# Kernel optimization log

Hardware: AMD Instinct MI355X
Metric: run time of the kernel (lower is better)

The kernel has to match this reference:

```python
import jax, jax.numpy as jnp
import numpy as np

N_BOND = 100000      # number of 'bond' nodes in the batched graph
IN_DIM = 32
SPACE_NUM = 6
D = SPACE_NUM * IN_DIM  # 192; bo_merge='cat' keeps h at space_num*in_dim
N_ETYPES = 36        # len(prot_atom_ids) * len(drug_atom_ids) = 4 * 9
E_PER_TYPE = 30000   # edges per edge type
B = 256              # batch_size (number of graphs)


def setup_inputs() -> dict:
    key = jax.random.key(0)
    k1, k2, k3, k4, k5 = jax.random.split(key, 5)
    h = jax.random.normal(k1, (N_BOND, D), dtype=jnp.float32)
    # output_layer: nn.Linear(D, 1, bias=False)
    W_out = jax.random.normal(k2, (D, 1), dtype=jnp.float32) / np.sqrt(D)
    # per-edge-type source node ids (DGL copy_u gather indices)
    edge_src = jax.random.randint(k3, (N_ETYPES, E_PER_TYPE), 0, N_BOND, dtype=jnp.int32)
    # per-edge graph id; sorted within each type (mimics arange(B).repeat(batch_num_edges))
    edge_seg = jnp.sort(jax.random.randint(k4, (N_ETYPES, E_PER_TYPE), 0, B, dtype=jnp.int32), axis=1)
    mask_mat = jax.random.randint(k5, (B, N_ETYPES), 0, 2).astype(bool)
    return {"h": h, "W_out": W_out, "edge_src": edge_src,
            "edge_seg": edge_seg, "mask_mat": mask_mat}


def reference(h, W_out, edge_src, edge_seg, mask_mat):
    # Fused over all 36 edge types: global segment id = type * B + graph_id
    type_idx = jnp.arange(N_ETYPES, dtype=edge_seg.dtype)[:, None]        # [T,1]
    seg_global = (type_idx * B + edge_seg).reshape(-1)                    # [T*E]
    eh = h[edge_src.reshape(-1)]                                          # gather: [T*E, D]
    sums = jax.ops.segment_sum(eh, seg_global, num_segments=N_ETYPES * B)  # [T*B, D]
    graph_feat = sums.reshape(N_ETYPES, B, D).transpose(1, 0, 2)          # [B, T, D]
    graph_v = jnp.einsum('btd,do->bt', graph_feat, W_out)                 # [B, T]
    graph_v = jnp.where(mask_mat, jnp.float32(-1e9), graph_v)
    return jax.nn.softmax(graph_v, axis=1)
```

## Files before the change

### kernel.cpp

```cpp
#include <hip/hip_runtime.h>

#define N_BOND   100000
#define D_DIM    192
#define N_ETYPES 36
#define E_PER_TYPE 30000
#define BATCH    256
#define TOTAL_E  (N_ETYPES * E_PER_TYPE)

__global__ void hv_kernel(const float* __restrict__ h, const float* __restrict__ W,
                          float* __restrict__ hv) {
    int gwave = (blockIdx.x * blockDim.x + threadIdx.x) >> 6;
    int lane  = threadIdx.x & 63;
    if (gwave >= N_BOND) return;
    float v = 0.f;
    if (lane < 48) {
        const float4 a = ((const float4*)(h + (size_t)gwave * D_DIM))[lane];
        const float4 w = ((const float4*)W)[lane];
        v = a.x * w.x + a.y * w.y + a.z * w.z + a.w * w.w;
    }
#pragma unroll
    for (int d = 32; d > 0; d >>= 1) v += __shfl_down(v, d, 64);
    if (lane == 0) hv[gwave] = v;
}

__global__ void edge_kernel(const int* __restrict__ edge_src,
                            const int* __restrict__ edge_seg,
                            const float* __restrict__ hv,
                            float* __restrict__ acc) {
    int e    = blockIdx.x * blockDim.x + threadIdx.x;
    int lane = threadIdx.x & 63;
    bool valid = (e < TOTAL_E);
    int ec  = valid ? e : (TOTAL_E - 1);
    int t   = ec / E_PER_TYPE;
    int seg = edge_seg[ec];
    int src = edge_src[ec];
    float val = valid ? hv[src] : 0.0f;
    int key = t * BATCH + seg;

#pragma unroll
    for (int d = 1; d < 64; d <<= 1) {
        float uv = __shfl_up(val, d, 64);
        int   uk = __shfl_up(key, d, 64);
        if (lane >= d && uk == key) val += uv;
    }
    int nk = __shfl_down(key, 1, 64);
    if (lane == 63 || nk != key) atomicAdd(&acc[key], val);
}

__global__ void softmax_kernel(const float* __restrict__ acc,
                               const void* __restrict__ mask,
                               float* __restrict__ out) {
    int b = threadIdx.x;

    const unsigned int* mi = (const unsigned int*)mask;
    bool is_u8 = false;
#pragma unroll
    for (int i = 0; i < 16; ++i) is_u8 |= (mi[i] > 1u);
    const unsigned char* m8  = (const unsigned char*)mask;
    const int*           m32 = (const int*)mask;

    float v[N_ETYPES];
    float mx = -1e30f;
#pragma unroll
    for (int t = 0; t < N_ETYPES; ++t) {
        float x = acc[t * BATCH + b];
        bool masked = is_u8 ? (m8[b * N_ETYPES + t] != 0)
                            : (m32[b * N_ETYPES + t] != 0);
        x = masked ? -1e9f : x;
        v[t] = x;
        mx = fmaxf(mx, x);
    }
    float s = 0.f;
#pragma unroll
    for (int t = 0; t < N_ETYPES; ++t) { v[t] = expf(v[t] - mx); s += v[t]; }
    float inv = 1.f / s;
#pragma unroll
    for (int t = 0; t < N_ETYPES; ++t) out[b * N_ETYPES + t] = v[t] * inv;
}

extern "C" void kernel_launch(void* const* d_in, const int* in_sizes, int n_in,
                              void* d_out, int out_size, void* d_ws, size_t ws_size,
                              hipStream_t stream) {
    const float* h        = (const float*)d_in[0];
    const float* W        = (const float*)d_in[1];
    const int*   edge_src = (const int*)d_in[2];
    const int*   edge_seg = (const int*)d_in[3];
    const void*  mask     = d_in[4];
    float*       out      = (float*)d_out;

    float* hv  = (float*)d_ws;
    float* acc = (float*)((char*)d_ws + 400128);

    hipMemsetAsync(acc, 0, N_ETYPES * BATCH * sizeof(float), stream);

    hipLaunchKernelGGL(hv_kernel, dim3((N_BOND + 3) / 4), dim3(256), 0, stream, h, W, hv);

    int eb = (TOTAL_E + 255) / 256;
    hipLaunchKernelGGL(edge_kernel, dim3(eb), dim3(256), 0, stream, edge_src, edge_seg, hv, acc);

    hipLaunchKernelGGL(softmax_kernel, dim3(1), dim3(256), 0, stream, acc, mask, out);
}
```

Before: 140.8 us.

## Fold acc zeroing into hv kernel and process 8 edges per thread serially

```diff
diff --git a/kernel.cpp b/kernel.cpp
--- a/kernel.cpp
+++ b/kernel.cpp
@@ -6,45 +6,51 @@
 #define E_PER_TYPE 30000
 #define BATCH    256
 #define TOTAL_E  (N_ETYPES * E_PER_TYPE)
+#define EPT      8
 
 __global__ void hv_kernel(const float* __restrict__ h, const float* __restrict__ W,
-                          float* __restrict__ hv) {
-    int gwave = (blockIdx.x * blockDim.x + threadIdx.x) >> 6;
-    int lane  = threadIdx.x & 63;
-    if (gwave >= N_BOND) return;
-    float v = 0.f;
-    if (lane < 48) {
-        const float4 a = ((const float4*)(h + (size_t)gwave * D_DIM))[lane];
-        const float4 w = ((const float4*)W)[lane];
-        v = a.x * w.x + a.y * w.y + a.z * w.z + a.w * w.w;
-    }
+                          float* __restrict__ hv, float* __restrict__ acc) {
+    int gid  = blockIdx.x * blockDim.x + threadIdx.x;
+    if (gid < N_ETYPES * BATCH) acc[gid] = 0.f;
+    int row  = gid >> 6;
+    int lane = threadIdx.x & 63;
+    if (row >= N_BOND) return;
+    const float* hr = h + (size_t)row * D_DIM;
+    float v = hr[lane]       * W[lane]
+            + hr[lane + 64]  * W[lane + 64]
+            + hr[lane + 128] * W[lane + 128];
 #pragma unroll
     for (int d = 32; d > 0; d >>= 1) v += __shfl_down(v, d, 64);
-    if (lane == 0) hv[gwave] = v;
+    if (lane == 0) hv[row] = v;
 }
 
 __global__ void edge_kernel(const int* __restrict__ edge_src,
                             const int* __restrict__ edge_seg,
                             const float* __restrict__ hv,
                             float* __restrict__ acc) {
-    int e    = blockIdx.x * blockDim.x + threadIdx.x;
-    int lane = threadIdx.x & 63;
-    bool valid = (e < TOTAL_E);
-    int ec  = valid ? e : (TOTAL_E - 1);
-    int t   = ec / E_PER_TYPE;
-    int seg = edge_seg[ec];
-    int src = edge_src[ec];
-    float val = valid ? hv[src] : 0.0f;
-    int key = t * BATCH + seg;
-
+    int tid  = blockIdx.x * blockDim.x + threadIdx.x;
+    int base = tid * EPT;
+    if (base >= TOTAL_E) return;
+    int t = base / E_PER_TYPE;
+    const int4* sp = (const int4*)(edge_src + base);
+    const int4* gp = (const int4*)(edge_seg + base);
+    int4 s0 = sp[0], s1 = sp[1];
+    int4 g0 = gp[0], g1 = gp[1];
+    int srcs[EPT] = {s0.x, s0.y, s0.z, s0.w, s1.x, s1.y, s1.z, s1.w};
+    int segs[EPT] = {g0.x, g0.y, g0.z, g0.w, g1.x, g1.y, g1.z, g1.w};
+    float vals[EPT];
 #pragma unroll
-    for (int d = 1; d < 64; d <<= 1) {
-        float uv = __shfl_up(val, d, 64);
-        int   uk = __shfl_up(key, d, 64);
-        if (lane >= d && uk == key) val += uv;
+    for (int j = 0; j < EPT; ++j) vals[j] = hv[srcs[j]];
+    int tb  = t * BATCH;
+    float run = vals[0];
+    int   rk  = tb + segs[0];
+#pragma unroll
+    for (int j = 1; j < EPT; ++j) {
+        int k = tb + segs[j];
+        if (k == rk) { run += vals[j]; }
+        else { atomicAdd(&acc[rk], run); rk = k; run = vals[j]; }
     }
-    int nk = __shfl_down(key, 1, 64);
-    if (lane == 63 || nk != key) atomicAdd(&acc[key], val);
+    atomicAdd(&acc[rk], run);
 }
 
 __global__ void softmax_kernel(const float* __restrict__ acc,
@@ -91,12 +97,12 @@
     float* hv  = (float*)d_ws;
     float* acc = (float*)((char*)d_ws + 400128);
 
-    hipMemsetAsync(acc, 0, N_ETYPES * BATCH * sizeof(float), stream);
+    hipLaunchKernelGGL(hv_kernel, dim3((N_BOND + 3) / 4), dim3(256), 0, stream,
+                       h, W, hv, acc);
 
-    hipLaunchKernelGGL(hv_kernel, dim3((N_BOND + 3) / 4), dim3(256), 0, stream, h, W, hv);
-
-    int eb = (TOTAL_E + 255) / 256;
-    hipLaunchKernelGGL(edge_kernel, dim3(eb), dim3(256), 0, stream, edge_src, edge_seg, hv, acc);
+    int nthreads = TOTAL_E / EPT;
+    hipLaunchKernelGGL(edge_kernel, dim3((nthreads + 255) / 256), dim3(256), 0, stream,
+                       edge_src, edge_seg, hv, acc);
 
     hipLaunchKernelGGL(softmax_kernel, dim3(1), dim3(256), 0, stream, acc, mask, out);
 }
```

Result: slower. 148.6 us (+5.5%).
